# Kernel optimization log

Measured on AMD Instinct MI355X. Metric: run time of the kernel, lower is better.

## Reference

```python
import jax, jax.numpy as jnp
import numpy as np

D_MODEL = 256; N_HEADS = 8; HEAD_DIM = 32; N_LEVELS = 4; N_POINTS = 4; N_LAYERS = 3; D_FFN = 1024
SHAPES = np.array([[76, 76], [38, 38], [19, 19], [10, 10]], dtype=np.int64)
S_TOTAL = int((SHAPES[:, 0] * SHAPES[:, 1]).sum())  # 7681


def setup_inputs():
    key = jax.random.key(0)
    ks = jax.random.split(key, 12)
    B = 1; C = D_MODEL; M = N_HEADS; Lv = N_LEVELS; P = N_POINTS; L = N_LAYERS; s = 0.02
    starts = np.concatenate([[0], np.cumsum(SHAPES[:, 0] * SHAPES[:, 1])[:-1]]).astype(np.int64)
    inp = {
        "src": jax.random.normal(ks[0], (B, S_TOTAL, C), jnp.float32),
        "pos": jax.random.normal(ks[1], (B, S_TOTAL, C), jnp.float32),
        "valid_ratios": jnp.ones((B, Lv, 2), jnp.float32),
        "spatial_shapes": jnp.asarray(SHAPES),
        "level_start_index": jnp.asarray(starts),
        "padding_mask": jnp.zeros((B, S_TOTAL), bool),
        "W_off": jax.random.normal(ks[2], (L, C, M * Lv * P * 2), jnp.float32) * s,
        "b_off": jax.random.normal(ks[3], (L, M * Lv * P * 2), jnp.float32) * s,
        "W_attn": jax.random.normal(ks[4], (L, C, M * Lv * P), jnp.float32) * s,
        "b_attn": jax.random.normal(ks[5], (L, M * Lv * P), jnp.float32) * s,
        "W_val": jax.random.normal(ks[6], (L, C, C), jnp.float32) * s,
        "b_val": jnp.zeros((L, C), jnp.float32),
        "W_out": jax.random.normal(ks[7], (L, C, C), jnp.float32) * s,
        "b_out": jnp.zeros((L, C), jnp.float32),
        "ln1_g": jnp.ones((L, C), jnp.float32),
        "ln1_b": jnp.zeros((L, C), jnp.float32),
        "W_ff1": jax.random.normal(ks[8], (L, C, D_FFN), jnp.float32) * s,
        "b_ff1": jnp.zeros((L, D_FFN), jnp.float32),
        "W_ff2": jax.random.normal(ks[9], (L, D_FFN, C), jnp.float32) * s,
        "b_ff2": jnp.zeros((L, C), jnp.float32),
        "ln2_g": jnp.ones((L, C), jnp.float32),
        "ln2_b": jnp.zeros((L, C), jnp.float32),
    }
    return inp


def _ln(x, g, b):
    mu = x.mean(-1, keepdims=True)
    var = ((x - mu) ** 2).mean(-1, keepdims=True)
    return (x - mu) * jax.lax.rsqrt(var + 1e-5) * g + b


def _gather(v, idx):
    # v: [B, HW, M, D], idx: [B, S, M, P] -> [B, S, M, P, D], head-specific gather
    B, S, M, P = idx.shape
    def one(vb, ib):
        i2 = ib.transpose(0, 2, 1).reshape(S * P, M, 1)
        o = jnp.take_along_axis(vb, i2, axis=0)  # [S*P, M, D]
        return o.reshape(S, P, M, -1).transpose(0, 2, 1, 3)
    return jax.vmap(one)(v, idx)


def _msda(query, src, mask, ref, shapes, starts, Wo, bo, Wa, ba, Wv, bv, Wout, bout):
    # Multi-scale deformable attention (Deformable-DETR), grid_sample align_corners=False + zero padding
    B, S, C = src.shape
    M, Lv, P, D = N_HEADS, N_LEVELS, N_POINTS, HEAD_DIM
    value = src @ Wv + bv
    value = jnp.where(mask[..., None], 0.0, value).reshape(B, S, M, D)
    off = (query @ Wo + bo).reshape(B, S, M, Lv, P, 2)
    aw = jax.nn.softmax((query @ Wa + ba).reshape(B, S, M, Lv * P), -1).reshape(B, S, M, Lv, P)
    norm = jnp.asarray(shapes[:, ::-1].copy(), jnp.float32)  # (W, H) per level
    loc = ref[:, :, None, :, None, :] + off / norm[None, None, None, :, None, :]  # [B,S,M,Lv,P,2]
    out = jnp.zeros((B, S, M, D), query.dtype)
    for lvl in range(Lv):
        H = int(shapes[lvl, 0]); W = int(shapes[lvl, 1]); st = int(starts[lvl])
        v = value[:, st:st + H * W]  # [B, H*W, M, D]
        l = loc[:, :, :, lvl]  # [B, S, M, P, 2]
        x = l[..., 0] * W - 0.5
        y = l[..., 1] * H - 0.5
        x0 = jnp.floor(x); y0 = jnp.floor(y)
        dx = x - x0; dy = y - y0
        samp = jnp.zeros((B, S, M, P, D), query.dtype)
        for yy, xx, w in ((y0, x0, (1 - dy) * (1 - dx)), (y0, x0 + 1, (1 - dy) * dx),
                          (y0 + 1, x0, dy * (1 - dx)), (y0 + 1, x0 + 1, dy * dx)):
            valid = (xx >= 0) & (xx < W) & (yy >= 0) & (yy < H)
            xi = jnp.clip(xx, 0, W - 1).astype(jnp.int32)
            yi = jnp.clip(yy, 0, H - 1).astype(jnp.int32)
            g = _gather(v, yi * W + xi)
            samp = samp + (w * valid)[..., None] * g
        out = out + (aw[:, :, :, lvl, :, None] * samp).sum(3)
    return out.reshape(B, S, C) @ Wout + bout


def _ref_points(vr, shapes):
    refs = []
    for lvl in range(shapes.shape[0]):
        H = int(shapes[lvl, 0]); W = int(shapes[lvl, 1])
        ry, rx = np.meshgrid(np.linspace(0.5, H - 0.5, H, dtype=np.float32),
                             np.linspace(0.5, W - 0.5, W, dtype=np.float32), indexing="ij")
        rxj = jnp.asarray(rx.reshape(-1))[None] / (vr[:, None, lvl, 0] * W)
        ryj = jnp.asarray(ry.reshape(-1))[None] / (vr[:, None, lvl, 1] * H)
        refs.append(jnp.stack([rxj, ryj], -1))
    ref = jnp.concatenate(refs, 1)  # [B, S, 2]
    return ref[:, :, None] * vr[:, None]  # [B, S, Lv, 2]


def _encoder(src, pos, valid_ratios, shapes, starts, mask, params):
    (W_off, b_off, W_attn, b_attn, W_val, b_val, W_out, b_out,
     ln1_g, ln1_b, W_ff1, b_ff1, W_ff2, b_ff2, ln2_g, ln2_b) = params
    ref = _ref_points(valid_ratios, shapes)
    out = src
    for l in range(N_LAYERS):
        q = out + pos  # with_pos_embed
        a = _msda(q, out, mask, ref, shapes, starts, W_off[l], b_off[l], W_attn[l], b_attn[l],
                  W_val[l], b_val[l], W_out[l], b_out[l])
        out = _ln(out + a, ln1_g[l], ln1_b[l])
        f = jax.nn.relu(out @ W_ff1[l] + b_ff1[l]) @ W_ff2[l] + b_ff2[l]
        out = _ln(out + f, ln2_g[l], ln2_b[l])
    return out


def reference(src, pos, valid_ratios, spatial_shapes, level_start_index, padding_mask,
              W_off, b_off, W_attn, b_attn, W_val, b_val, W_out, b_out,
              ln1_g, ln1_b, W_ff1, b_ff1, W_ff2, b_ff2, ln2_g, ln2_b):
    shapes = np.asarray(spatial_shapes)
    starts = np.asarray(level_start_index)
    params = (W_off, b_off, W_attn, b_attn, W_val, b_val, W_out, b_out,
              ln1_g, ln1_b, W_ff1, b_ff1, W_ff2, b_ff2, ln2_g, ln2_b)
    return _encoder(src, pos, valid_ratios, shapes, starts, padding_mask, params)
```

## Files before the change

### kernel.cpp

```cpp
#include <hip/hip_runtime.h>
#include <hip/hip_bf16.h>
#include <math.h>

#define S_TOTAL 7681

typedef __attribute__((ext_vector_type(8))) short bf16x8;
typedef __attribute__((ext_vector_type(4))) float f32x4;

__device__ __forceinline__ short f2b(float x) {
    union { float f; unsigned u; } v; v.f = x;
    unsigned r = v.u + 0x7FFFu + ((v.u >> 16) & 1u);
    return (short)(r >> 16);
}
__device__ __forceinline__ float b2f(unsigned short u) {
    union { unsigned u; float f; } t; t.u = ((unsigned)u) << 16; return t.f;
}

__device__ __forceinline__ void gll16(const short* g, short* l) {
    __builtin_amdgcn_global_load_lds(
        (const __attribute__((address_space(1))) unsigned int*)g,
        (__attribute__((address_space(3))) unsigned int*)l,
        16, 0, 0);
}

#define SBAR() asm volatile("s_barrier" ::: "memory")

#define MFMA16(a, b, c) __builtin_amdgcn_mfma_f32_16x16x32_bf16(a, b, c, 0, 0, 0)

__global__ __launch_bounds__(256) void transpose_cvt_kernel(
    const float* __restrict__ s0, const float* __restrict__ s1,
    const float* __restrict__ s2, const float* __restrict__ s3,
    const float* __restrict__ s4, const float* __restrict__ s5,
    short* __restrict__ d0, short* __restrict__ d1, short* __restrict__ d2,
    short* __restrict__ d3, short* __restrict__ d4, short* __restrict__ d5,
    const float4* __restrict__ csrc, const float4* __restrict__ cpos,
    float4* __restrict__ co, ushort4* __restrict__ cxb, ushort4* __restrict__ cqb)
{
    const int z = blockIdx.z;
    int t = blockIdx.x;
    if (t >= 736) {
        const int n4 = S_TOTAL * 64;
        int i = (z * 641 + (t - 736)) * 256 + threadIdx.x;
        if (i < n4) {
            float4 v = csrc[i], p = cpos[i];
            co[i] = v;
            ushort4 h, hq;
            h.x = (unsigned short)f2b(v.x); h.y = (unsigned short)f2b(v.y);
            h.z = (unsigned short)f2b(v.z); h.w = (unsigned short)f2b(v.w);
            hq.x = (unsigned short)f2b(v.x + p.x); hq.y = (unsigned short)f2b(v.y + p.y);
            hq.z = (unsigned short)f2b(v.z + p.z); hq.w = (unsigned short)f2b(v.w + p.w);
            cxb[i] = h;
            cqb[i] = hq;
        }
        return;
    }
    const float* src; short* dst; int K, N, lt;
    if (t < 64)       { src = s0 + (size_t)z * 65536;  dst = d0 + (size_t)z * 65536;  K = 256;  N = 256;  lt = t; }
    else if (t < 128) { src = s1 + (size_t)z * 65536;  dst = d1 + (size_t)z * 98304;  K = 256;  N = 256;  lt = t - 64; }
    else if (t < 160) { src = s2 + (size_t)z * 32768;  dst = d2 + (size_t)z * 98304;  K = 256;  N = 128;  lt = t - 128; }
    else if (t < 224) { src = s3 + (size_t)z * 65536;  dst = d3 + (size_t)z * 65536;  K = 256;  N = 256;  lt = t - 160; }
    else if (t < 480) { src = s4 + (size_t)z * 262144; dst = d4 + (size_t)z * 262144; K = 256;  N = 1024; lt = t - 224; }
    else              { src = s5 + (size_t)z * 262144; dst = d5 + (size_t)z * 262144; K = 1024; N = 256;  lt = t - 480; }
    const int ntx = N >> 5;
    const int tk = (lt / ntx) << 5, tn = (lt % ntx) << 5;
    __shared__ float tile[32][33];
    const int cx = threadIdx.x & 31, cy = threadIdx.x >> 5;
    #pragma unroll
    for (int i = 0; i < 32; i += 8)
        tile[cy + i][cx] = src[(size_t)(tk + cy + i) * N + tn + cx];
    __syncthreads();
    #pragma unroll
    for (int i = 0; i < 32; i += 8)
        dst[(size_t)(tn + cy + i) * K + tk + cx] = f2b(tile[cx][cy + i]);
}


__global__ __launch_bounds__(256) void gemm_va_kernel(
    const short* __restrict__ xb, const short* __restrict__ qb,
    const short* __restrict__ Wt_val, const short* __restrict__ Wt_oa,
    const float* __restrict__ b_val, const float* __restrict__ b_off,
    const float* __restrict__ b_attn,
    short* __restrict__ value_bf, float* __restrict__ offbuf, int M)
{
    const int grp = (blockIdx.y >= 4);
    const short* A  = grp ? qb : xb;
    const short* Wt = grp ? Wt_oa : Wt_val;
    const int colBase = (grp ? (blockIdx.y - 4) : blockIdx.y) * 64;
    const int K = 256;

    __shared__ __align__(16) short As[2][128 * 64];
    __shared__ __align__(16) short Bs[2][64 * 64];

    const int tid = threadIdx.x;
    const int lane = tid & 63;
    const int wave = tid >> 6;
    const int rowBase = blockIdx.x * 128;

    const int sr = lane >> 3;
    const int sc = ((lane & 7) ^ sr) << 3;

    const short* gA[4];
    #pragma unroll
    for (int c = 0; c < 4; ++c)
        gA[c] = A + (size_t)min(rowBase + wave * 32 + c * 8 + sr, M - 1) * K + sc;
    const short* gB[2];
    #pragma unroll
    for (int c = 0; c < 2; ++c)
        gB[c] = Wt + (size_t)(colBase + wave * 16 + c * 8 + sr) * K + sc;

    const int frow = lane & 15;
    const int g4 = lane >> 4;
    const int r7 = frow & 7;
    const int wm = wave * 32;

    f32x4 acc[2][4] = {};

    auto stage = [&](int buf, int k0) {
        #pragma unroll
        for (int c = 0; c < 4; ++c)
            gll16(gA[c] + k0, &As[buf][(wave * 32 + c * 8) * 64]);
        #pragma unroll
        for (int c = 0; c < 2; ++c)
            gll16(gB[c] + k0, &Bs[buf][(wave * 16 + c * 8) * 64]);
    };

    stage(0, 0);

    int cur = 0;
    for (int k0 = 0; k0 < K; k0 += 64) {
        if (k0 + 64 < K) {
            stage(cur ^ 1, k0 + 64);
            asm volatile("s_waitcnt vmcnt(6)" ::: "memory");
        } else {
            asm volatile("s_waitcnt vmcnt(0)" ::: "memory");
        }
        SBAR();
        #pragma unroll
        for (int kk8 = 0; kk8 < 8; kk8 += 4) {
            const int ua = (((kk8 + g4) ^ r7) << 3);
            bf16x8 af0 = *(const bf16x8*)&As[cur][(wm + frow) * 64 + ua];
            bf16x8 af1 = *(const bf16x8*)&As[cur][(wm + 16 + frow) * 64 + ua];
            #pragma unroll
            for (int j = 0; j < 4; ++j) {
                bf16x8 bfj = *(const bf16x8*)&Bs[cur][(j * 16 + frow) * 64 + ua];
                acc[0][j] = MFMA16(af0, bfj, acc[0][j]);
                acc[1][j] = MFMA16(af1, bfj, acc[1][j]);
            }
        }
        SBAR();
        cur ^= 1;
    }

    const int erow = (lane >> 4) * 4;
    const int ecol = lane & 15;
    #pragma unroll
    for (int mi = 0; mi < 2; ++mi) {
        #pragma unroll
        for (int j = 0; j < 4; ++j) {
            int col = colBase + j * 16 + ecol;
            float bias = grp ? (col < 256 ? b_off[col] : b_attn[col - 256]) : b_val[col];
            #pragma unroll
            for (int r = 0; r < 4; ++r) {
                int row = rowBase + wm + mi * 16 + erow + r;
                if (row < M) {
                    float v = acc[mi][j][r] + bias;
                    if (grp) offbuf[(size_t)row * 384 + col] = v;
                    else     value_bf[(size_t)row * 256 + col] = f2b(v);
                }
            }
        }
    }
}

template<int RELU, int OUTBF>
__global__ __launch_bounds__(256) void gemm_kernel(
    const short* __restrict__ A, const short* __restrict__ Wt,
    const float* __restrict__ bias, void* __restrict__ Cv,
    int M, int N, int K)
{
    __shared__ __align__(16) short As[2][128 * 64];
    __shared__ __align__(16) short Bs[2][64 * 64];

    const int tid = threadIdx.x;
    const int lane = tid & 63;
    const int wave = tid >> 6;
    const int rowBase = blockIdx.x * 128;
    const int colBase = blockIdx.y * 64;

    const int sr = lane >> 3;
    const int sc = ((lane & 7) ^ sr) << 3;

    const short* gA[4];
    #pragma unroll
    for (int c = 0; c < 4; ++c)
        gA[c] = A + (size_t)min(rowBase + wave * 32 + c * 8 + sr, M - 1) * K + sc;
    const short* gB[2];
    #pragma unroll
    for (int c = 0; c < 2; ++c)
        gB[c] = Wt + (size_t)(colBase + wave * 16 + c * 8 + sr) * K + sc;

    const int frow = lane & 15;
    const int g4 = lane >> 4;
    const int r7 = frow & 7;
    const int wm = wave * 32;

    f32x4 acc[2][4] = {};

    auto stage = [&](int buf, int k0) {
        #pragma unroll
        for (int c = 0; c < 4; ++c)
            gll16(gA[c] + k0, &As[buf][(wave * 32 + c * 8) * 64]);
        #pragma unroll
        for (int c = 0; c < 2; ++c)
            gll16(gB[c] + k0, &Bs[buf][(wave * 16 + c * 8) * 64]);
    };

    stage(0, 0);

    int cur = 0;
    for (int k0 = 0; k0 < K; k0 += 64) {
        if (k0 + 64 < K) {
            stage(cur ^ 1, k0 + 64);
            asm volatile("s_waitcnt vmcnt(6)" ::: "memory");
        } else {
            asm volatile("s_waitcnt vmcnt(0)" ::: "memory");
        }
        SBAR();
        #pragma unroll
        for (int kk8 = 0; kk8 < 8; kk8 += 4) {
            const int ua = (((kk8 + g4) ^ r7) << 3);
            bf16x8 af0 = *(const bf16x8*)&As[cur][(wm + frow) * 64 + ua];
            bf16x8 af1 = *(const bf16x8*)&As[cur][(wm + 16 + frow) * 64 + ua];
            #pragma unroll
            for (int j = 0; j < 4; ++j) {
                bf16x8 bfj = *(const bf16x8*)&Bs[cur][(j * 16 + frow) * 64 + ua];
                acc[0][j] = MFMA16(af0, bfj, acc[0][j]);
                acc[1][j] = MFMA16(af1, bfj, acc[1][j]);
            }
        }
        SBAR();
        cur ^= 1;
    }

    const int erow = (lane >> 4) * 4;
    const int ecol = lane & 15;
    #pragma unroll
    for (int mi = 0; mi < 2; ++mi) {
        #pragma unroll
        for (int j = 0; j < 4; ++j) {
            #pragma unroll
            for (int r = 0; r < 4; ++r) {
                int row = rowBase + wm + mi * 16 + erow + r;
                if (row < M) {
                    int col = colBase + j * 16 + ecol;
                    float v = acc[mi][j][r] + bias[col];
                    if (RELU) v = fmaxf(v, 0.f);
                    if (OUTBF) ((short*)Cv)[(size_t)row * N + col] = f2b(v);
                    else       ((float*)Cv)[(size_t)row * N + col] = v;
                }
            }
        }
    }
}

template<int WRITEQ>
__global__ __launch_bounds__(256) void gemm_ln_kernel(
    const short* __restrict__ A, const short* __restrict__ Wt,
    const float* __restrict__ bias, const float* __restrict__ g,
    const float* __restrict__ bln, const float* __restrict__ pos,
    float* __restrict__ out, short* __restrict__ xb, short* __restrict__ qb,
    int M, int K)
{
    __shared__ __align__(16) short As[2][16 * 64];
    __shared__ __align__(16) short Bs[2][256 * 64];
    __shared__ float rsum[16][4], rsq[16][4], smu[16], srs[16];

    const int tid = threadIdx.x;
    const int lane = tid & 63;
    const int wave = tid >> 6;
    const int rowBase = blockIdx.x * 16;

    const int sr = lane >> 3;
    const int sc = ((lane & 7) ^ sr) << 3;

    const short* gA = A + (size_t)min(rowBase + wave * 8 + sr, M - 1) * K + sc;
    const short* gB[8];
    #pragma unroll
    for (int c = 0; c < 8; ++c)
        gB[c] = Wt + (size_t)(wave * 64 + c * 8 + sr) * K + sc;

    const int frow = lane & 15;
    const int g4 = lane >> 4;
    const int r7 = frow & 7;

    f32x4 acc[4] = {};

    auto stage = [&](int buf, int k0) {
        if (wave < 2) gll16(gA + k0, &As[buf][(wave * 8) * 64]);
        #pragma unroll
        for (int c = 0; c < 8; ++c)
            gll16(gB[c] + k0, &Bs[buf][(wave * 64 + c * 8) * 64]);
    };

    stage(0, 0);

    int cur = 0;
    for (int k0 = 0; k0 < K; k0 += 64) {
        if (k0 + 64 < K) {
            stage(cur ^ 1, k0 + 64);
            if (wave < 2) asm volatile("s_waitcnt vmcnt(9)" ::: "memory");
            else          asm volatile("s_waitcnt vmcnt(8)" ::: "memory");
        } else {
            asm volatile("s_waitcnt vmcnt(0)" ::: "memory");
        }
        SBAR();
        #pragma unroll
        for (int kk8 = 0; kk8 < 8; kk8 += 4) {
            const int ua = (((kk8 + g4) ^ r7) << 3);
            bf16x8 af = *(const bf16x8*)&As[cur][frow * 64 + ua];
            #pragma unroll
            for (int j = 0; j < 4; ++j) {
                bf16x8 bfj = *(const bf16x8*)&Bs[cur][(wave * 64 + j * 16 + frow) * 64 + ua];
                acc[j] = MFMA16(af, bfj, acc[j]);
            }
        }
        SBAR();
        cur ^= 1;
    }

    const int erow = (lane >> 4) * 4;
    const int ecol = lane & 15;
    float x[4][4];
    #pragma unroll
    for (int j = 0; j < 4; ++j)
        #pragma unroll
        for (int r = 0; r < 4; ++r) {
            int row = rowBase + erow + r;
            int col = wave * 64 + j * 16 + ecol;
            float res = (row < M) ? out[(size_t)row * 256 + col] : 0.f;
            x[j][r] = acc[j][r] + bias[col] + res;
        }

    #pragma unroll
    for (int r = 0; r < 4; ++r) {
        float s1 = x[0][r] + x[1][r] + x[2][r] + x[3][r];
        float s2 = x[0][r]*x[0][r] + x[1][r]*x[1][r]
                 + x[2][r]*x[2][r] + x[3][r]*x[3][r];
        #pragma unroll
        for (int o = 1; o < 16; o <<= 1) {
            s1 += __shfl_xor(s1, o);
            s2 += __shfl_xor(s2, o);
        }
        if ((lane & 15) == 0) {
            rsum[erow + r][wave] = s1;
            rsq [erow + r][wave] = s2;
        }
    }
    __syncthreads();
    if (tid < 16) {
        float S1 = rsum[tid][0] + rsum[tid][1] + rsum[tid][2] + rsum[tid][3];
        float S2 = rsq[tid][0] + rsq[tid][1] + rsq[tid][2] + rsq[tid][3];
        float mu = S1 * (1.f / 256.f);
        smu[tid] = mu;
        srs[tid] = rsqrtf(S2 * (1.f / 256.f) - mu * mu + 1e-5f);
    }
    __syncthreads();

    #pragma unroll
    for (int r = 0; r < 4; ++r) {
        int lrow = erow + r;
        int row = rowBase + lrow;
        if (row >= M) continue;
        float mu = smu[lrow], rs = srs[lrow];
        #pragma unroll
        for (int j = 0; j < 4; ++j) {
            int col = wave * 64 + j * 16 + ecol;
            float y = (x[j][r] - mu) * rs * g[col] + bln[col];
            out[(size_t)row * 256 + col] = y;
            xb[(size_t)row * 256 + col] = f2b(y);
            if (WRITEQ)
                qb[(size_t)row * 256 + col] = f2b(y + pos[(size_t)row * 256 + col]);
        }
    }
}

__global__ __launch_bounds__(256) void msda_kernel(
    const short* __restrict__ value, const float* __restrict__ offb,
    short* __restrict__ msdab)
{
    __shared__ float   soff[8 * 384];
    __shared__ ushort4 sIdx[1024];
    __shared__ float4  sWgt[1024];

    const int bid = blockIdx.x;
    const int sb = (bid & 7) * 121 + (bid >> 3);
    const int q0 = sb * 8;
    if (q0 >= S_TOTAL) return;
    const int tid = threadIdx.x;

    {
        const float4* src4 = (const float4*)offb;
        #pragma unroll
        for (int i = tid; i < 768; i += 256) {
            int qi = i / 96, j = i - qi * 96;
            int q = min(q0 + qi, S_TOTAL - 1);
            *(float4*)&soff[qi * 384 + j * 4] = src4[(size_t)q * 96 + j];
        }
    }
    __syncthreads();

    if (tid < 64) {
        const int qi = tid >> 3, m = tid & 7;
        float* lg = &soff[qi * 384 + 256 + m * 16];
        float mx = -1e30f;
        #pragma unroll
        for (int k = 0; k < 16; ++k) mx = fmaxf(mx, lg[k]);
        float e[16], sum = 0.f;
        #pragma unroll
        for (int k = 0; k < 16; ++k) { e[k] = expf(lg[k] - mx); sum += e[k]; }
        float inv = 1.f / sum;
        #pragma unroll
        for (int k = 0; k < 16; ++k) lg[k] = e[k] * inv;
    }
    __syncthreads();

    #pragma unroll
    for (int it = tid; it < 1024; it += 256) {
        const int qi = it >> 7, i = it & 127;
        const int lvl = (i >> 2) & 3;
        const int q = min(q0 + qi, S_TOTAL - 1);

        float refx, refy;
        if (q < 5776)      { int t = q;        int r = t / 76, c = t % 76; refx = (c + 0.5f) / 76.f; refy = (r + 0.5f) / 76.f; }
        else if (q < 7220) { int t = q - 5776; int r = t / 38, c = t % 38; refx = (c + 0.5f) / 38.f; refy = (r + 0.5f) / 38.f; }
        else if (q < 7581) { int t = q - 7220; int r = t / 19, c = t % 19; refx = (c + 0.5f) / 19.f; refy = (r + 0.5f) / 19.f; }
        else               { int t = q - 7581; int r = t / 10, c = t % 10; refx = (c + 0.5f) / 10.f; refy = (r + 0.5f) / 10.f; }

        const int LVL_HW[4] = {76, 38, 19, 10};
        const int LVL_ST[4] = {0, 5776, 7220, 7581};
        const int W = LVL_HW[lvl];
        const float fW = (float)W;

        float ox = soff[qi * 384 + i * 2];
        float oy = soff[qi * 384 + i * 2 + 1];
        float aw = soff[qi * 384 + 256 + i];

        float x = refx * fW + ox - 0.5f;
        float y = refy * fW + oy - 0.5f;
        float x0f = floorf(x), y0f = floorf(y);
        int x0 = (int)x0f, y0 = (int)y0f;
        float dx = x - x0f, dy = y - y0f;

        bool vx0 = (x0 >= 0) & (x0 < W);
        bool vx1 = (x0 >= -1) & (x0 < W - 1);
        bool vy0 = (y0 >= 0) & (y0 < W);
        bool vy1 = (y0 >= -1) & (y0 < W - 1);
        int xc0 = min(max(x0, 0), W - 1), xc1 = min(max(x0 + 1, 0), W - 1);
        int yc0 = min(max(y0, 0), W - 1), yc1 = min(max(y0 + 1, 0), W - 1);
        int base = LVL_ST[lvl];
        ushort4 id;
        id.x = (unsigned short)(base + yc0 * W + xc0);
        id.y = (unsigned short)(base + yc0 * W + xc1);
        id.z = (unsigned short)(base + yc1 * W + xc0);
        id.w = (unsigned short)(base + yc1 * W + xc1);
        float4 w4;
        w4.x = (vy0 && vx0) ? (1.f - dy) * (1.f - dx) * aw : 0.f;
        w4.y = (vy0 && vx1) ? (1.f - dy) * dx * aw : 0.f;
        w4.z = (vy1 && vx0) ? dy * (1.f - dx) * aw : 0.f;
        w4.w = (vy1 && vx1) ? dy * dx * aw : 0.f;
        sIdx[it] = id;
        sWgt[it] = w4;
    }
    __syncthreads();

    const int lane = tid & 63;
    const int qi = (tid >> 6) * 2 + (lane >> 5);
    const int q = q0 + qi;
    if (q >= S_TOTAL) return;
    const int l32 = lane & 31;
    const int h = l32 >> 2, dg = l32 & 3;
    const short* vcol = value + h * 32 + dg * 8;
    const int itb = qi * 128 + (h << 4);

    float a[8] = {};
    #pragma unroll
    for (int pt = 0; pt < 16; ++pt) {
        const ushort4 id = sIdx[itb + pt];
        const float4 w = sWgt[itb + pt];
        bf16x8 v0 = *(const bf16x8*)(vcol + ((size_t)id.x << 8));
        bf16x8 v1 = *(const bf16x8*)(vcol + ((size_t)id.y << 8));
        bf16x8 v2 = *(const bf16x8*)(vcol + ((size_t)id.z << 8));
        bf16x8 v3 = *(const bf16x8*)(vcol + ((size_t)id.w << 8));
        #pragma unroll
        for (int e = 0; e < 8; ++e)
            a[e] += w.x * b2f((unsigned short)v0[e]) + w.y * b2f((unsigned short)v1[e])
                  + w.z * b2f((unsigned short)v2[e]) + w.w * b2f((unsigned short)v3[e]);
    }
    bf16x8 o;
    #pragma unroll
    for (int e = 0; e < 8; ++e) o[e] = f2b(a[e]);
    *(bf16x8*)(msdab + (size_t)q * 256 + h * 32 + dg * 8) = o;
}

extern "C" void kernel_launch(void* const* d_in, const int* in_sizes, int n_in,
                              void* d_out, int out_size, void* d_ws, size_t ws_size,
                              hipStream_t stream) {
    const float* src    = (const float*)d_in[0];
    const float* pos    = (const float*)d_in[1];
    const float* W_off  = (const float*)d_in[6];
    const float* b_off  = (const float*)d_in[7];
    const float* W_attn = (const float*)d_in[8];
    const float* b_attn = (const float*)d_in[9];
    const float* W_val  = (const float*)d_in[10];
    const float* b_val  = (const float*)d_in[11];
    const float* W_out  = (const float*)d_in[12];
    const float* b_out  = (const float*)d_in[13];
    const float* ln1_g  = (const float*)d_in[14];
    const float* ln1_b  = (const float*)d_in[15];
    const float* W_ff1  = (const float*)d_in[16];
    const float* b_ff1  = (const float*)d_in[17];
    const float* W_ff2  = (const float*)d_in[18];
    const float* b_ff2  = (const float*)d_in[19];
    const float* ln2_g  = (const float*)d_in[20];
    const float* ln2_b  = (const float*)d_in[21];

    const size_t S = S_TOTAL;
    float* out = (float*)d_out;

    short* wt = (short*)d_ws;
    short* Wt_val = wt;
    short* Wt_oa  = wt + 196608;
    short* Wt_out = wt + 491520;
    short* Wt_ff1 = wt + 688128;
    short* Wt_ff2 = wt + 1474560;
    float* fbase  = (float*)d_ws + 1131648;
    short* xb       = (short*)fbase;
    short* qb       = (short*)(fbase + 128 * S);
    short* value_bf = (short*)(fbase + 256 * S);
    float* offb     = fbase + 384 * S;
    short* msdab    = (short*)(fbase + 768 * S);
    short* hid      = (short*)(fbase + 256 * S);

    transpose_cvt_kernel<<<dim3(1377, 1, 3), 256, 0, stream>>>(
        W_val, W_off, W_attn, W_out, W_ff1, W_ff2,
        Wt_val, Wt_oa, Wt_oa + 65536, Wt_out, Wt_ff1, Wt_ff2,
        (const float4*)src, (const float4*)pos,
        (float4*)out, (ushort4*)xb, (ushort4*)qb);

    const int MB = (S_TOTAL + 127) / 128;
    const int LB = (S_TOTAL + 15) / 16;

    for (int l = 0; l < 3; ++l) {
        gemm_va_kernel<<<dim3(MB, 10), 256, 0, stream>>>(
            xb, qb, Wt_val + (size_t)l * 65536, Wt_oa + (size_t)l * 98304,
            b_val + (size_t)l * 256, b_off + (size_t)l * 256, b_attn + (size_t)l * 128,
            value_bf, offb, S_TOTAL);
        msda_kernel<<<968, 256, 0, stream>>>(value_bf, offb, msdab);
        gemm_ln_kernel<0><<<LB, 256, 0, stream>>>(
            msdab, Wt_out + (size_t)l * 65536, b_out + (size_t)l * 256,
            ln1_g + (size_t)l * 256, ln1_b + (size_t)l * 256, pos,
            out, xb, qb, S_TOTAL, 256);
        gemm_kernel<1, 1><<<dim3(MB, 16), 256, 0, stream>>>(
            xb, Wt_ff1 + (size_t)l * 262144, b_ff1 + (size_t)l * 1024, hid,
            S_TOTAL, 1024, 256);
        gemm_ln_kernel<1><<<LB, 256, 0, stream>>>(
            hid, Wt_ff2 + (size_t)l * 262144, b_ff2 + (size_t)l * 256,
            ln2_g + (size_t)l * 256, ln2_b + (size_t)l * 256, pos,
            out, xb, qb, S_TOTAL, 1024);
    }
}
```

Baseline: 367.5 us.

## Fuse out-proj+LN1, FFN1, FFN2+LN2 into one per-16-row tail kernel

```diff
diff --git a/kernel.cpp b/kernel.cpp
--- a/kernel.cpp
+++ b/kernel.cpp
@@ -74,7 +74,6 @@
         dst[(size_t)(tn + cy + i) * K + tk + cx] = f2b(tile[cx][cy + i]);
 }
 
-
 __global__ __launch_bounds__(256) void gemm_va_kernel(
     const short* __restrict__ xb, const short* __restrict__ qb,
     const short* __restrict__ Wt_val, const short* __restrict__ Wt_oa,
@@ -172,107 +171,24 @@
     }
 }
 
-template<int RELU, int OUTBF>
-__global__ __launch_bounds__(256) void gemm_kernel(
-    const short* __restrict__ A, const short* __restrict__ Wt,
-    const float* __restrict__ bias, void* __restrict__ Cv,
-    int M, int N, int K)
+__global__ __launch_bounds__(256) void fused_tail_kernel(
+    const short* __restrict__ A,
+    const short* __restrict__ Wt_out,
+    const float* __restrict__ b_out,
+    const float* __restrict__ g1, const float* __restrict__ bl1,
+    const short* __restrict__ Wt_f1,
+    const float* __restrict__ b_f1,
+    const short* __restrict__ Wt_f2,
+    const float* __restrict__ b_f2,
+    const float* __restrict__ g2, const float* __restrict__ bl2,
+    const float* __restrict__ pos,
+    float* __restrict__ out, short* __restrict__ xb, short* __restrict__ qb,
+    int M)
 {
-    __shared__ __align__(16) short As[2][128 * 64];
-    __shared__ __align__(16) short Bs[2][64 * 64];
-
-    const int tid = threadIdx.x;
-    const int lane = tid & 63;
-    const int wave = tid >> 6;
-    const int rowBase = blockIdx.x * 128;
-    const int colBase = blockIdx.y * 64;
-
-    const int sr = lane >> 3;
-    const int sc = ((lane & 7) ^ sr) << 3;
-
-    const short* gA[4];
-    #pragma unroll
-    for (int c = 0; c < 4; ++c)
-        gA[c] = A + (size_t)min(rowBase + wave * 32 + c * 8 + sr, M - 1) * K + sc;
-    const short* gB[2];
-    #pragma unroll
-    for (int c = 0; c < 2; ++c)
-        gB[c] = Wt + (size_t)(colBase + wave * 16 + c * 8 + sr) * K + sc;
-
-    const int frow = lane & 15;
-    const int g4 = lane >> 4;
-    const int r7 = frow & 7;
-    const int wm = wave * 32;
-
-    f32x4 acc[2][4] = {};
-
-    auto stage = [&](int buf, int k0) {
-        #pragma unroll
-        for (int c = 0; c < 4; ++c)
-            gll16(gA[c] + k0, &As[buf][(wave * 32 + c * 8) * 64]);
-        #pragma unroll
-        for (int c = 0; c < 2; ++c)
-            gll16(gB[c] + k0, &Bs[buf][(wave * 16 + c * 8) * 64]);
-    };
-
-    stage(0, 0);
-
-    int cur = 0;
-    for (int k0 = 0; k0 < K; k0 += 64) {
-        if (k0 + 64 < K) {
-            stage(cur ^ 1, k0 + 64);
-            asm volatile("s_waitcnt vmcnt(6)" ::: "memory");
-        } else {
-            asm volatile("s_waitcnt vmcnt(0)" ::: "memory");
-        }
-        SBAR();
-        #pragma unroll
-        for (int kk8 = 0; kk8 < 8; kk8 += 4) {
-            const int ua = (((kk8 + g4) ^ r7) << 3);
-            bf16x8 af0 = *(const bf16x8*)&As[cur][(wm + frow) * 64 + ua];
-            bf16x8 af1 = *(const bf16x8*)&As[cur][(wm + 16 + frow) * 64 + ua];
-            #pragma unroll
-            for (int j = 0; j < 4; ++j) {
-                bf16x8 bfj = *(const bf16x8*)&Bs[cur][(j * 16 + frow) * 64 + ua];
-                acc[0][j] = MFMA16(af0, bfj, acc[0][j]);
-                acc[1][j] = MFMA16(af1, bfj, acc[1][j]);
-            }
-        }
-        SBAR();
-        cur ^= 1;
-    }
-
-    const int erow = (lane >> 4) * 4;
-    const int ecol = lane & 15;
-    #pragma unroll
-    for (int mi = 0; mi < 2; ++mi) {
-        #pragma unroll
-        for (int j = 0; j < 4; ++j) {
-            #pragma unroll
-            for (int r = 0; r < 4; ++r) {
-                int row = rowBase + wm + mi * 16 + erow + r;
-                if (row < M) {
-                    int col = colBase + j * 16 + ecol;
-                    float v = acc[mi][j][r] + bias[col];
-                    if (RELU) v = fmaxf(v, 0.f);
-                    if (OUTBF) ((short*)Cv)[(size_t)row * N + col] = f2b(v);
-                    else       ((float*)Cv)[(size_t)row * N + col] = v;
-                }
-            }
-        }
-    }
-}
-
-template<int WRITEQ>
-__global__ __launch_bounds__(256) void gemm_ln_kernel(
-    const short* __restrict__ A, const short* __restrict__ Wt,
-    const float* __restrict__ bias, const float* __restrict__ g,
-    const float* __restrict__ bln, const float* __restrict__ pos,
-    float* __restrict__ out, short* __restrict__ xb, short* __restrict__ qb,
-    int M, int K)
-{
-    __shared__ __align__(16) short As[2][16 * 64];
+    __shared__ __align__(16) short As1[2][16 * 64];
     __shared__ __align__(16) short Bs[2][256 * 64];
+    __shared__ __align__(16) short a1[16 * 256];
+    __shared__ __align__(16) short hid[16 * 1024];
     __shared__ float rsum[16][4], rsq[16][4], smu[16], srs[16];
 
     const int tid = threadIdx.x;
@@ -283,103 +199,236 @@
     const int sr = lane >> 3;
     const int sc = ((lane & 7) ^ sr) << 3;
 
-    const short* gA = A + (size_t)min(rowBase + wave * 8 + sr, M - 1) * K + sc;
-    const short* gB[8];
-    #pragma unroll
-    for (int c = 0; c < 8; ++c)
-        gB[c] = Wt + (size_t)(wave * 64 + c * 8 + sr) * K + sc;
+    const short* gA  = A + (size_t)min(rowBase + wave * 8 + sr, M - 1) * 256 + sc;
+    const short* gB1 = Wt_out + (size_t)(wave * 64 + sr) * 256 + sc;
+    const short* gB2 = Wt_f1  + (size_t)(wave * 64 + sr) * 256 + sc;
+    const short* gB3 = Wt_f2  + (size_t)(wave * 64 + sr) * 1024 + sc;
 
     const int frow = lane & 15;
     const int g4 = lane >> 4;
     const int r7 = frow & 7;
+    const int erow = g4 * 4;
+    const int ecol = frow;
 
     f32x4 acc[4] = {};
-
-    auto stage = [&](int buf, int k0) {
-        if (wave < 2) gll16(gA + k0, &As[buf][(wave * 8) * 64]);
+    {
+        if (wave < 2) gll16(gA, &As1[0][wave * 8 * 64]);
         #pragma unroll
         for (int c = 0; c < 8; ++c)
-            gll16(gB[c] + k0, &Bs[buf][(wave * 64 + c * 8) * 64]);
-    };
-
-    stage(0, 0);
-
-    int cur = 0;
-    for (int k0 = 0; k0 < K; k0 += 64) {
-        if (k0 + 64 < K) {
-            stage(cur ^ 1, k0 + 64);
-            if (wave < 2) asm volatile("s_waitcnt vmcnt(9)" ::: "memory");
-            else          asm volatile("s_waitcnt vmcnt(8)" ::: "memory");
-        } else {
-            asm volatile("s_waitcnt vmcnt(0)" ::: "memory");
-        }
-        SBAR();
-        #pragma unroll
-        for (int kk8 = 0; kk8 < 8; kk8 += 4) {
-            const int ua = (((kk8 + g4) ^ r7) << 3);
-            bf16x8 af = *(const bf16x8*)&As[cur][frow * 64 + ua];
+            gll16(gB1 + c * 8 * 256, &Bs[0][(wave * 64 + c * 8) * 64]);
+
+        int cur = 0;
+        #pragma unroll
+        for (int k0 = 0; k0 < 256; k0 += 64) {
+            if (k0 + 64 < 256) {
+                if (wave < 2) gll16(gA + k0 + 64, &As1[cur ^ 1][wave * 8 * 64]);
+                #pragma unroll
+                for (int c = 0; c < 8; ++c)
+                    gll16(gB1 + c * 8 * 256 + k0 + 64, &Bs[cur ^ 1][(wave * 64 + c * 8) * 64]);
+                if (wave < 2) asm volatile("s_waitcnt vmcnt(9)" ::: "memory");
+                else          asm volatile("s_waitcnt vmcnt(8)" ::: "memory");
+            } else {
+                asm volatile("s_waitcnt vmcnt(0)" ::: "memory");
+            }
+            SBAR();
+            #pragma unroll
+            for (int kk8 = 0; kk8 < 8; kk8 += 4) {
+                const int ua = (((kk8 + g4) ^ r7) << 3);
+                bf16x8 af = *(const bf16x8*)&As1[cur][frow * 64 + ua];
+                #pragma unroll
+                for (int j = 0; j < 4; ++j) {
+                    bf16x8 bfj = *(const bf16x8*)&Bs[cur][(wave * 64 + j * 16 + frow) * 64 + ua];
+                    acc[j] = MFMA16(af, bfj, acc[j]);
+                }
+            }
+            SBAR();
+            cur ^= 1;
+        }
+    }
+
+    float y1[4][4];
+    {
+        float x[4][4];
+        #pragma unroll
+        for (int j = 0; j < 4; ++j)
+            #pragma unroll
+            for (int r = 0; r < 4; ++r) {
+                int row = rowBase + erow + r;
+                int col = wave * 64 + j * 16 + ecol;
+                float res = (row < M) ? out[(size_t)row * 256 + col] : 0.f;
+                x[j][r] = acc[j][r] + b_out[col] + res;
+            }
+        #pragma unroll
+        for (int r = 0; r < 4; ++r) {
+            float s1 = x[0][r] + x[1][r] + x[2][r] + x[3][r];
+            float s2 = x[0][r]*x[0][r] + x[1][r]*x[1][r]
+                     + x[2][r]*x[2][r] + x[3][r]*x[3][r];
+            #pragma unroll
+            for (int o = 1; o < 16; o <<= 1) {
+                s1 += __shfl_xor(s1, o);
+                s2 += __shfl_xor(s2, o);
+            }
+            if ((lane & 15) == 0) {
+                rsum[erow + r][wave] = s1;
+                rsq [erow + r][wave] = s2;
+            }
+        }
+        __syncthreads();
+        if (tid < 16) {
+            float S1 = rsum[tid][0] + rsum[tid][1] + rsum[tid][2] + rsum[tid][3];
+            float S2 = rsq[tid][0] + rsq[tid][1] + rsq[tid][2] + rsq[tid][3];
+            float mu = S1 * (1.f / 256.f);
+            smu[tid] = mu;
+            srs[tid] = rsqrtf(S2 * (1.f / 256.f) - mu * mu + 1e-5f);
+        }
+        __syncthreads();
+        #pragma unroll
+        for (int j = 0; j < 4; ++j)
+            #pragma unroll
+            for (int r = 0; r < 4; ++r) {
+                int lrow = erow + r;
+                int col = wave * 64 + j * 16 + ecol;
+                float yv = (x[j][r] - smu[lrow]) * srs[lrow] * g1[col] + bl1[col];
+                y1[j][r] = yv;
+                int u = col >> 3;
+                int usw = u ^ (lrow & 7);
+                a1[lrow * 256 + usw * 8 + (col & 7)] = f2b(yv);
+            }
+    }
+    __syncthreads();
+
+    {
+        #pragma unroll
+        for (int c = 0; c < 8; ++c)
+            gll16(gB2 + c * 2048, &Bs[0][(wave * 64 + c * 8) * 64]);
+
+        int cur = 0;
+        #pragma unroll
+        for (int nc = 0; nc < 4; ++nc) {
+            f32x4 acc2[4] = {};
+            #pragma unroll
+            for (int kc = 0; kc < 4; ++kc) {
+                const int s = nc * 4 + kc;
+                if (s + 1 < 16) {
+                    const int nn = (s + 1) >> 2, kk = (s + 1) & 3;
+                    #pragma unroll
+                    for (int c = 0; c < 8; ++c)
+                        gll16(gB2 + nn * 65536 + c * 2048 + kk * 64,
+                              &Bs[cur ^ 1][(wave * 64 + c * 8) * 64]);
+                    asm volatile("s_waitcnt vmcnt(8)" ::: "memory");
+                } else {
+                    asm volatile("s_waitcnt vmcnt(0)" ::: "memory");
+                }
+                SBAR();
+                #pragma unroll
+                for (int kk8 = 0; kk8 < 8; kk8 += 4) {
+                    const int lu = (kk8 + g4) ^ r7;
+                    bf16x8 af = *(const bf16x8*)&a1[frow * 256 + (kc * 8 + lu) * 8];
+                    #pragma unroll
+                    for (int j = 0; j < 4; ++j) {
+                        bf16x8 bfj = *(const bf16x8*)&Bs[cur][(wave * 64 + j * 16 + frow) * 64 + (lu << 3)];
+                        acc2[j] = MFMA16(af, bfj, acc2[j]);
+                    }
+                }
+                SBAR();
+                cur ^= 1;
+            }
             #pragma unroll
             for (int j = 0; j < 4; ++j) {
-                bf16x8 bfj = *(const bf16x8*)&Bs[cur][(wave * 64 + j * 16 + frow) * 64 + ua];
-                acc[j] = MFMA16(af, bfj, acc[j]);
-            }
-        }
-        SBAR();
-        cur ^= 1;
-    }
-
-    const int erow = (lane >> 4) * 4;
-    const int ecol = lane & 15;
-    float x[4][4];
-    #pragma unroll
-    for (int j = 0; j < 4; ++j)
+                int col = nc * 256 + wave * 64 + j * 16 + ecol;
+                float bias = b_f1[col];
+                #pragma unroll
+                for (int r = 0; r < 4; ++r) {
+                    int lrow = erow + r;
+                    float v = fmaxf(acc2[j][r] + bias, 0.f);
+                    int u = col >> 3;
+                    int usw = (u & ~7) | ((u ^ lrow) & 7);
+                    hid[lrow * 1024 + usw * 8 + (col & 7)] = f2b(v);
+                }
+            }
+        }
+    }
+    __syncthreads();
+
+    f32x4 acc3[4] = {};
+    {
+        #pragma unroll
+        for (int c = 0; c < 8; ++c)
+            gll16(gB3 + c * 8192, &Bs[0][(wave * 64 + c * 8) * 64]);
+
+        int cur = 0;
+        for (int k0 = 0; k0 < 1024; k0 += 64) {
+            if (k0 + 64 < 1024) {
+                #pragma unroll
+                for (int c = 0; c < 8; ++c)
+                    gll16(gB3 + c * 8192 + k0 + 64, &Bs[cur ^ 1][(wave * 64 + c * 8) * 64]);
+                asm volatile("s_waitcnt vmcnt(8)" ::: "memory");
+            } else {
+                asm volatile("s_waitcnt vmcnt(0)" ::: "memory");
+            }
+            SBAR();
+            #pragma unroll
+            for (int kk8 = 0; kk8 < 8; kk8 += 4) {
+                const int lu = (kk8 + g4) ^ r7;
+                bf16x8 af = *(const bf16x8*)&hid[frow * 1024 + ((k0 >> 3) + lu) * 8];
+                #pragma unroll
+                for (int j = 0; j < 4; ++j) {
+                    bf16x8 bfj = *(const bf16x8*)&Bs[cur][(wave * 64 + j * 16 + frow) * 64 + (lu << 3)];
+                    acc3[j] = MFMA16(af, bfj, acc3[j]);
+                }
+            }
+            SBAR();
+            cur ^= 1;
+        }
+    }
+
+    {
+        float x[4][4];
+        #pragma unroll
+        for (int j = 0; j < 4; ++j)
+            #pragma unroll
+            for (int r = 0; r < 4; ++r) {
+                int col = wave * 64 + j * 16 + ecol;
+                x[j][r] = acc3[j][r] + b_f2[col] + y1[j][r];
+            }
         #pragma unroll
         for (int r = 0; r < 4; ++r) {
-            int row = rowBase + erow + r;
-            int col = wave * 64 + j * 16 + ecol;
-            float res = (row < M) ? out[(size_t)row * 256 + col] : 0.f;
-            x[j][r] = acc[j][r] + bias[col] + res;
-        }
-
-    #pragma unroll
-    for (int r = 0; r < 4; ++r) {
-        float s1 = x[0][r] + x[1][r] + x[2][r] + x[3][r];
-        float s2 = x[0][r]*x[0][r] + x[1][r]*x[1][r]
-                 + x[2][r]*x[2][r] + x[3][r]*x[3][r];
-        #pragma unroll
-        for (int o = 1; o < 16; o <<= 1) {
-            s1 += __shfl_xor(s1, o);
-            s2 += __shfl_xor(s2, o);
-        }
-        if ((lane & 15) == 0) {
-            rsum[erow + r][wave] = s1;
-            rsq [erow + r][wave] = s2;
-        }
-    }
-    __syncthreads();
-    if (tid < 16) {
-        float S1 = rsum[tid][0] + rsum[tid][1] + rsum[tid][2] + rsum[tid][3];
-        float S2 = rsq[tid][0] + rsq[tid][1] + rsq[tid][2] + rsq[tid][3];
-        float mu = S1 * (1.f / 256.f);
-        smu[tid] = mu;
-        srs[tid] = rsqrtf(S2 * (1.f / 256.f) - mu * mu + 1e-5f);
-    }
-    __syncthreads();
-
-    #pragma unroll
-    for (int r = 0; r < 4; ++r) {
-        int lrow = erow + r;
-        int row = rowBase + lrow;
-        if (row >= M) continue;
-        float mu = smu[lrow], rs = srs[lrow];
-        #pragma unroll
-        for (int j = 0; j < 4; ++j) {
-            int col = wave * 64 + j * 16 + ecol;
-            float y = (x[j][r] - mu) * rs * g[col] + bln[col];
-            out[(size_t)row * 256 + col] = y;
-            xb[(size_t)row * 256 + col] = f2b(y);
-            if (WRITEQ)
+            float s1 = x[0][r] + x[1][r] + x[2][r] + x[3][r];
+            float s2 = x[0][r]*x[0][r] + x[1][r]*x[1][r]
+                     + x[2][r]*x[2][r] + x[3][r]*x[3][r];
+            #pragma unroll
+            for (int o = 1; o < 16; o <<= 1) {
+                s1 += __shfl_xor(s1, o);
+                s2 += __shfl_xor(s2, o);
+            }
+            if ((lane & 15) == 0) {
+                rsum[erow + r][wave] = s1;
+                rsq [erow + r][wave] = s2;
+            }
+        }
+        __syncthreads();
+        if (tid < 16) {
+            float S1 = rsum[tid][0] + rsum[tid][1] + rsum[tid][2] + rsum[tid][3];
+            float S2 = rsq[tid][0] + rsq[tid][1] + rsq[tid][2] + rsq[tid][3];
+            float mu = S1 * (1.f / 256.f);
+            smu[tid] = mu;
+            srs[tid] = rsqrtf(S2 * (1.f / 256.f) - mu * mu + 1e-5f);
+        }
+        __syncthreads();
+        #pragma unroll
+        for (int r = 0; r < 4; ++r) {
+            int lrow = erow + r;
+            int row = rowBase + lrow;
+            if (row >= M) continue;
+            float mu = smu[lrow], rs = srs[lrow];
+            #pragma unroll
+            for (int j = 0; j < 4; ++j) {
+                int col = wave * 64 + j * 16 + ecol;
+                float y = (x[j][r] - mu) * rs * g2[col] + bl2[col];
+                out[(size_t)row * 256 + col] = y;
+                xb[(size_t)row * 256 + col] = f2b(y);
                 qb[(size_t)row * 256 + col] = f2b(y + pos[(size_t)row * 256 + col]);
+            }
         }
     }
 }
@@ -539,7 +588,6 @@
     short* value_bf = (short*)(fbase + 256 * S);
     float* offb     = fbase + 384 * S;
     short* msdab    = (short*)(fbase + 768 * S);
-    short* hid      = (short*)(fbase + 256 * S);
 
     transpose_cvt_kernel<<<dim3(1377, 1, 3), 256, 0, stream>>>(
         W_val, W_off, W_attn, W_out, W_ff1, W_ff2,
@@ -556,16 +604,12 @@
             b_val + (size_t)l * 256, b_off + (size_t)l * 256, b_attn + (size_t)l * 128,
             value_bf, offb, S_TOTAL);
         msda_kernel<<<968, 256, 0, stream>>>(value_bf, offb, msdab);
-        gemm_ln_kernel<0><<<LB, 256, 0, stream>>>(
+        fused_tail_kernel<<<LB, 256, 0, stream>>>(
             msdab, Wt_out + (size_t)l * 65536, b_out + (size_t)l * 256,
-            ln1_g + (size_t)l * 256, ln1_b + (size_t)l * 256, pos,
-            out, xb, qb, S_TOTAL, 256);
-        gemm_kernel<1, 1><<<dim3(MB, 16), 256, 0, stream>>>(
-            xb, Wt_ff1 + (size_t)l * 262144, b_ff1 + (size_t)l * 1024, hid,
-            S_TOTAL, 1024, 256);
-        gemm_ln_kernel<1><<<LB, 256, 0, stream>>>(
-            hid, Wt_ff2 + (size_t)l * 262144, b_ff2 + (size_t)l * 256,
-            ln2_g + (size_t)l * 256, ln2_b + (size_t)l * 256, pos,
-            out, xb, qb, S_TOTAL, 1024);
-    }
-}
+            ln1_g + (size_t)l * 256, ln1_b + (size_t)l * 256,
+            Wt_ff1 + (size_t)l * 262144, b_ff1 + (size_t)l * 1024,
+            Wt_ff2 + (size_t)l * 262144, b_ff2 + (size_t)l * 256,
+            ln2_g + (size_t)l * 256, ln2_b + (size_t)l * 256,
+            pos, out, xb, qb, S_TOTAL);
+    }
+}
```

Measured after the change: 391.3 us. 1.06x slower.

## Split GEMM+LayerNorm into generic tiled GEMM with residual and separate LN kernel

Applied to the files above, without the earlier changes.

```diff
diff --git a/kernel.cpp b/kernel.cpp
--- a/kernel.cpp
+++ b/kernel.cpp
@@ -74,7 +74,6 @@
         dst[(size_t)(tn + cy + i) * K + tk + cx] = f2b(tile[cx][cy + i]);
 }
 
-
 __global__ __launch_bounds__(256) void gemm_va_kernel(
     const short* __restrict__ xb, const short* __restrict__ qb,
     const short* __restrict__ Wt_val, const short* __restrict__ Wt_oa,
@@ -172,11 +171,11 @@
     }
 }
 
-template<int RELU, int OUTBF>
+template<int RELU, int OUTBF, int RESID>
 __global__ __launch_bounds__(256) void gemm_kernel(
     const short* __restrict__ A, const short* __restrict__ Wt,
-    const float* __restrict__ bias, void* __restrict__ Cv,
-    int M, int N, int K)
+    const float* __restrict__ bias, const float* __restrict__ resid,
+    void* __restrict__ Cv, int M, int N, int K)
 {
     __shared__ __align__(16) short As[2][128 * 64];
     __shared__ __align__(16) short Bs[2][64 * 64];
@@ -254,6 +253,7 @@
                 if (row < M) {
                     int col = colBase + j * 16 + ecol;
                     float v = acc[mi][j][r] + bias[col];
+                    if (RESID) v += resid[(size_t)row * N + col];
                     if (RELU) v = fmaxf(v, 0.f);
                     if (OUTBF) ((short*)Cv)[(size_t)row * N + col] = f2b(v);
                     else       ((float*)Cv)[(size_t)row * N + col] = v;
@@ -264,123 +264,46 @@
 }
 
 template<int WRITEQ>
-__global__ __launch_bounds__(256) void gemm_ln_kernel(
-    const short* __restrict__ A, const short* __restrict__ Wt,
-    const float* __restrict__ bias, const float* __restrict__ g,
-    const float* __restrict__ bln, const float* __restrict__ pos,
-    float* __restrict__ out, short* __restrict__ xb, short* __restrict__ qb,
-    int M, int K)
+__global__ __launch_bounds__(256) void ln_kernel(
+    const float4* __restrict__ tmp, const float4* __restrict__ g4v,
+    const float4* __restrict__ b4v, const float4* __restrict__ pos,
+    float4* __restrict__ out, ushort4* __restrict__ xb, ushort4* __restrict__ qb,
+    int M)
 {
-    __shared__ __align__(16) short As[2][16 * 64];
-    __shared__ __align__(16) short Bs[2][256 * 64];
-    __shared__ float rsum[16][4], rsq[16][4], smu[16], srs[16];
-
-    const int tid = threadIdx.x;
-    const int lane = tid & 63;
-    const int wave = tid >> 6;
-    const int rowBase = blockIdx.x * 16;
-
-    const int sr = lane >> 3;
-    const int sc = ((lane & 7) ^ sr) << 3;
-
-    const short* gA = A + (size_t)min(rowBase + wave * 8 + sr, M - 1) * K + sc;
-    const short* gB[8];
-    #pragma unroll
-    for (int c = 0; c < 8; ++c)
-        gB[c] = Wt + (size_t)(wave * 64 + c * 8 + sr) * K + sc;
-
-    const int frow = lane & 15;
-    const int g4 = lane >> 4;
-    const int r7 = frow & 7;
-
-    f32x4 acc[4] = {};
-
-    auto stage = [&](int buf, int k0) {
-        if (wave < 2) gll16(gA + k0, &As[buf][(wave * 8) * 64]);
-        #pragma unroll
-        for (int c = 0; c < 8; ++c)
-            gll16(gB[c] + k0, &Bs[buf][(wave * 64 + c * 8) * 64]);
-    };
-
-    stage(0, 0);
-
-    int cur = 0;
-    for (int k0 = 0; k0 < K; k0 += 64) {
-        if (k0 + 64 < K) {
-            stage(cur ^ 1, k0 + 64);
-            if (wave < 2) asm volatile("s_waitcnt vmcnt(9)" ::: "memory");
-            else          asm volatile("s_waitcnt vmcnt(8)" ::: "memory");
-        } else {
-            asm volatile("s_waitcnt vmcnt(0)" ::: "memory");
-        }
-        SBAR();
-        #pragma unroll
-        for (int kk8 = 0; kk8 < 8; kk8 += 4) {
-            const int ua = (((kk8 + g4) ^ r7) << 3);
-            bf16x8 af = *(const bf16x8*)&As[cur][frow * 64 + ua];
-            #pragma unroll
-            for (int j = 0; j < 4; ++j) {
-                bf16x8 bfj = *(const bf16x8*)&Bs[cur][(wave * 64 + j * 16 + frow) * 64 + ua];
-                acc[j] = MFMA16(af, bfj, acc[j]);
-            }
-        }
-        SBAR();
-        cur ^= 1;
-    }
-
-    const int erow = (lane >> 4) * 4;
-    const int ecol = lane & 15;
-    float x[4][4];
-    #pragma unroll
-    for (int j = 0; j < 4; ++j)
-        #pragma unroll
-        for (int r = 0; r < 4; ++r) {
-            int row = rowBase + erow + r;
-            int col = wave * 64 + j * 16 + ecol;
-            float res = (row < M) ? out[(size_t)row * 256 + col] : 0.f;
-            x[j][r] = acc[j][r] + bias[col] + res;
-        }
-
-    #pragma unroll
-    for (int r = 0; r < 4; ++r) {
-        float s1 = x[0][r] + x[1][r] + x[2][r] + x[3][r];
-        float s2 = x[0][r]*x[0][r] + x[1][r]*x[1][r]
-                 + x[2][r]*x[2][r] + x[3][r]*x[3][r];
-        #pragma unroll
-        for (int o = 1; o < 16; o <<= 1) {
-            s1 += __shfl_xor(s1, o);
-            s2 += __shfl_xor(s2, o);
-        }
-        if ((lane & 15) == 0) {
-            rsum[erow + r][wave] = s1;
-            rsq [erow + r][wave] = s2;
-        }
-    }
-    __syncthreads();
-    if (tid < 16) {
-        float S1 = rsum[tid][0] + rsum[tid][1] + rsum[tid][2] + rsum[tid][3];
-        float S2 = rsq[tid][0] + rsq[tid][1] + rsq[tid][2] + rsq[tid][3];
-        float mu = S1 * (1.f / 256.f);
-        smu[tid] = mu;
-        srs[tid] = rsqrtf(S2 * (1.f / 256.f) - mu * mu + 1e-5f);
-    }
-    __syncthreads();
-
-    #pragma unroll
-    for (int r = 0; r < 4; ++r) {
-        int lrow = erow + r;
-        int row = rowBase + lrow;
-        if (row >= M) continue;
-        float mu = smu[lrow], rs = srs[lrow];
-        #pragma unroll
-        for (int j = 0; j < 4; ++j) {
-            int col = wave * 64 + j * 16 + ecol;
-            float y = (x[j][r] - mu) * rs * g[col] + bln[col];
-            out[(size_t)row * 256 + col] = y;
-            xb[(size_t)row * 256 + col] = f2b(y);
-            if (WRITEQ)
-                qb[(size_t)row * 256 + col] = f2b(y + pos[(size_t)row * 256 + col]);
-        }
+    const int lane = threadIdx.x & 63;
+    const int row = blockIdx.x * 4 + (threadIdx.x >> 6);
+    if (row >= M) return;
+    const size_t idx = (size_t)row * 64 + lane;
+
+    float4 v = tmp[idx];
+    float s1 = v.x + v.y + v.z + v.w;
+    float s2 = v.x * v.x + v.y * v.y + v.z * v.z + v.w * v.w;
+    #pragma unroll
+    for (int o = 1; o < 64; o <<= 1) {
+        s1 += __shfl_xor(s1, o);
+        s2 += __shfl_xor(s2, o);
+    }
+    float mu = s1 * (1.f / 256.f);
+    float rs = rsqrtf(s2 * (1.f / 256.f) - mu * mu + 1e-5f);
+
+    float4 gg = g4v[lane], bb = b4v[lane];
+    float4 y;
+    y.x = (v.x - mu) * rs * gg.x + bb.x;
+    y.y = (v.y - mu) * rs * gg.y + bb.y;
+    y.z = (v.z - mu) * rs * gg.z + bb.z;
+    y.w = (v.w - mu) * rs * gg.w + bb.w;
+
+    out[idx] = y;
+    ushort4 h;
+    h.x = (unsigned short)f2b(y.x); h.y = (unsigned short)f2b(y.y);
+    h.z = (unsigned short)f2b(y.z); h.w = (unsigned short)f2b(y.w);
+    xb[idx] = h;
+    if (WRITEQ) {
+        float4 p = pos[idx];
+        ushort4 hq;
+        hq.x = (unsigned short)f2b(y.x + p.x); hq.y = (unsigned short)f2b(y.y + p.y);
+        hq.z = (unsigned short)f2b(y.z + p.z); hq.w = (unsigned short)f2b(y.w + p.w);
+        qb[idx] = hq;
     }
 }
 
@@ -539,6 +462,7 @@
     short* value_bf = (short*)(fbase + 256 * S);
     float* offb     = fbase + 384 * S;
     short* msdab    = (short*)(fbase + 768 * S);
+    float* tmp      = fbase + 896 * S;
     short* hid      = (short*)(fbase + 256 * S);
 
     transpose_cvt_kernel<<<dim3(1377, 1, 3), 256, 0, stream>>>(
@@ -548,7 +472,7 @@
         (float4*)out, (ushort4*)xb, (ushort4*)qb);
 
     const int MB = (S_TOTAL + 127) / 128;
-    const int LB = (S_TOTAL + 15) / 16;
+    const int LNB = (S_TOTAL + 3) / 4;
 
     for (int l = 0; l < 3; ++l) {
         gemm_va_kernel<<<dim3(MB, 10), 256, 0, stream>>>(
@@ -556,16 +480,22 @@
             b_val + (size_t)l * 256, b_off + (size_t)l * 256, b_attn + (size_t)l * 128,
             value_bf, offb, S_TOTAL);
         msda_kernel<<<968, 256, 0, stream>>>(value_bf, offb, msdab);
-        gemm_ln_kernel<0><<<LB, 256, 0, stream>>>(
+        gemm_kernel<0, 0, 1><<<dim3(MB, 4), 256, 0, stream>>>(
             msdab, Wt_out + (size_t)l * 65536, b_out + (size_t)l * 256,
-            ln1_g + (size_t)l * 256, ln1_b + (size_t)l * 256, pos,
-            out, xb, qb, S_TOTAL, 256);
-        gemm_kernel<1, 1><<<dim3(MB, 16), 256, 0, stream>>>(
-            xb, Wt_ff1 + (size_t)l * 262144, b_ff1 + (size_t)l * 1024, hid,
-            S_TOTAL, 1024, 256);
-        gemm_ln_kernel<1><<<LB, 256, 0, stream>>>(
+            out, tmp, S_TOTAL, 256, 256);
+        ln_kernel<0><<<LNB, 256, 0, stream>>>(
+            (const float4*)tmp, (const float4*)(ln1_g + (size_t)l * 256),
+            (const float4*)(ln1_b + (size_t)l * 256), (const float4*)pos,
+            (float4*)out, (ushort4*)xb, (ushort4*)qb, S_TOTAL);
+        gemm_kernel<1, 1, 0><<<dim3(MB, 16), 256, 0, stream>>>(
+            xb, Wt_ff1 + (size_t)l * 262144, b_ff1 + (size_t)l * 1024,
+            nullptr, hid, S_TOTAL, 1024, 256);
+        gemm_kernel<0, 0, 1><<<dim3(MB, 4), 256, 0, stream>>>(
             hid, Wt_ff2 + (size_t)l * 262144, b_ff2 + (size_t)l * 256,
-            ln2_g + (size_t)l * 256, ln2_b + (size_t)l * 256, pos,
-            out, xb, qb, S_TOTAL, 1024);
-    }
-}
+            out, tmp, S_TOTAL, 256, 1024);
+        ln_kernel<1><<<LNB, 256, 0, stream>>>(
+            (const float4*)tmp, (const float4*)(ln2_g + (size_t)l * 256),
+            (const float4*)(ln2_b + (size_t)l * 256), (const float4*)pos,
+            (float4*)out, (ushort4*)xb, (ushort4*)qb, S_TOTAL);
+    }
+}
```

Measured after the change: 427.7 us. 1.16x slower.
